# Optimization experiments

Hardware: AMD Instinct MI355X
Metric: run time of the kernel (lower is better)

## Reference

```python
import jax, jax.numpy as jnp
import numpy as np

N = 50000        # nodes
E = 800000       # edges (avg degree 16)
IN = 256         # in_size
H = 4            # heads
C = 32           # out_size per head
NEG_SLOPE = 0.2  # PyG GATConv leaky_relu slope
LN_EPS = 1e-5


def setup_inputs() -> dict:
    key = jax.random.key(0)
    ks = jax.random.split(key, 6)
    x = jax.random.normal(ks[0], (N, IN), dtype=jnp.float32)
    edge_index = jax.random.randint(ks[1], (2, E), 0, N, dtype=jnp.int32)
    W = jax.random.normal(ks[2], (IN, H * C), dtype=jnp.float32) * 0.05
    att_src = jax.random.normal(ks[3], (H, C), dtype=jnp.float32) * 0.05
    att_dst = jax.random.normal(ks[4], (H, C), dtype=jnp.float32) * 0.05
    bias = jnp.zeros((H * C,), dtype=jnp.float32)
    ln_gamma = jnp.ones((H * C,), dtype=jnp.float32)
    ln_beta = jnp.zeros((H * C,), dtype=jnp.float32)
    return {"x": x, "edge_index": edge_index, "W": W, "att_src": att_src,
            "att_dst": att_dst, "bias": bias, "ln_gamma": ln_gamma,
            "ln_beta": ln_beta}


def _segment_softmax(alpha, seg, num_segments):
    # alpha: [E, H], softmax over edges sharing the same destination node.
    amax = jax.ops.segment_max(alpha, seg, num_segments=num_segments)  # [N, H]
    amax = jnp.where(jnp.isfinite(amax), amax, 0.0)  # nodes with no in-edges
    ex = jnp.exp(alpha - amax[seg])
    denom = jax.ops.segment_sum(ex, seg, num_segments=num_segments)    # [N, H]
    return ex / (denom[seg] + 1e-16)


def reference(x, edge_index, W, att_src, att_dst, bias, ln_gamma, ln_beta):
    # --- GATConv (concat=True) ---
    x_lin = (x @ W).reshape(N, H, C)                    # [N, H, C]
    a_src = jnp.sum(x_lin * att_src, axis=-1)           # [N, H]
    a_dst = jnp.sum(x_lin * att_dst, axis=-1)           # [N, H]
    src, dst = edge_index[0], edge_index[1]             # messages src -> dst
    alpha = a_src[src] + a_dst[dst]                     # [E, H]
    alpha = jnp.where(alpha >= 0, alpha, NEG_SLOPE * alpha)
    alpha = _segment_softmax(alpha, dst, N)             # [E, H]
    msg = x_lin[src] * alpha[..., None]                 # [E, H, C]
    out = jax.ops.segment_sum(msg, dst, num_segments=N) # [N, H, C]
    out = out.reshape(N, H * C) + bias                  # [N, H*C]
    # --- LayerNorm over feature dim ---
    mu = jnp.mean(out, axis=-1, keepdims=True)
    var = jnp.mean(jnp.square(out - mu), axis=-1, keepdims=True)
    out = (out - mu) * jax.lax.rsqrt(var + LN_EPS) * ln_gamma + ln_beta
    # --- activation ---
    return jax.nn.relu(out)
```

## Files before the change

kernel.cpp:

```cpp
#include <hip/hip_runtime.h>

#define NNODES 50000
#define NEDGES 800000
#define INFEAT 256
#define HC 128
#define NH 4
#define CPH 32

typedef unsigned int uint32;
typedef unsigned short u16;
typedef short short8 __attribute__((ext_vector_type(8)));
typedef float f32x4 __attribute__((ext_vector_type(4)));

__device__ __forceinline__ float b2f(u16 s) {
    uint32 u = ((uint32)s) << 16;
    return __builtin_bit_cast(float, u);
}
__device__ __forceinline__ u16 f2bf(float x) {
    uint32 u = __builtin_bit_cast(uint32, x);
    uint32 r = (u + 0x7FFFu + ((u >> 16) & 1u)) >> 16;
    return (u16)r;
}
__device__ __forceinline__ uint32 pkh2(float a, float b) {
    _Float16 ha = (_Float16)a, hb = (_Float16)b;
    uint32 ua = (uint32)__builtin_bit_cast(unsigned short, ha);
    uint32 ub = (uint32)__builtin_bit_cast(unsigned short, hb);
    return ua | (ub << 16);
}
__device__ __forceinline__ float h2f(u16 h) {
    return (float)__builtin_bit_cast(_Float16, h);
}
__device__ __forceinline__ bool probe_bf16(const void* gamma) {
    return ((const uint32*)gamma)[0] == 0x3F803F80u;
}

__global__ __launch_bounds__(256) void wt_kernel(const void* __restrict__ W,
                                                 const void* __restrict__ gm,
                                                 u16* __restrict__ wt) {
    const bool isbf = probe_bf16(gm);
    int n = blockIdx.x;
    int k = threadIdx.x;
    u16 v;
    if (isbf) v = ((const u16*)W)[k * HC + n];
    else      v = f2bf(((const float*)W)[k * HC + n]);
    wt[n * INFEAT + k] = v;
}

__global__ __launch_bounds__(256) void gemm_mfma(const void* __restrict__ x,
                                                 const u16* __restrict__ wt,
                                                 const void* __restrict__ gm,
                                                 u16* __restrict__ xlin) {
    const bool isbf = probe_bf16(gm);
    int wave = blockIdx.x * 4 + (threadIdx.x >> 6);
    int lane = threadIdx.x & 63;
    int r = lane & 15;
    int quad = lane >> 4;
    int m0 = wave * 16;
    int arow = m0 + r;
    if (arow > NNODES - 1) arow = NNODES - 1;
    const size_t abase = (size_t)arow * INFEAT + quad * 8;

    f32x4 acc[8];
#pragma unroll
    for (int nt = 0; nt < 8; ++nt) acc[nt] = (f32x4){0.f, 0.f, 0.f, 0.f};

#pragma unroll
    for (int kt = 0; kt < 8; ++kt) {
        const int k0 = kt * 32;
        short8 afrag;
        if (isbf) {
            uint4 q = *(const uint4*)((const u16*)x + abase + k0);
            afrag = __builtin_bit_cast(short8, q);
        } else {
            const float* xp = (const float*)x + abase + k0;
            float4 f0 = *(const float4*)xp;
            float4 f1 = *(const float4*)(xp + 4);
            uint4 q;
            q.x = (uint32)f2bf(f0.x) | ((uint32)f2bf(f0.y) << 16);
            q.y = (uint32)f2bf(f0.z) | ((uint32)f2bf(f0.w) << 16);
            q.z = (uint32)f2bf(f1.x) | ((uint32)f2bf(f1.y) << 16);
            q.w = (uint32)f2bf(f1.z) | ((uint32)f2bf(f1.w) << 16);
            afrag = __builtin_bit_cast(short8, q);
        }
#pragma unroll
        for (int nt = 0; nt < 8; ++nt) {
            uint4 qb = *(const uint4*)(wt + (size_t)(nt * 16 + r) * INFEAT + k0 + quad * 8);
            short8 bfrag = __builtin_bit_cast(short8, qb);
            acc[nt] = __builtin_amdgcn_mfma_f32_16x16x32_bf16(afrag, bfrag, acc[nt], 0, 0, 0);
        }
    }
#pragma unroll
    for (int nt = 0; nt < 8; ++nt) {
#pragma unroll
        for (int reg = 0; reg < 4; ++reg) {
            int grow = m0 + quad * 4 + reg;
            if (grow < NNODES) xlin[(size_t)grow * HC + nt * 16 + r] = f2bf(acc[nt][reg]);
        }
    }
}

__global__ __launch_bounds__(256) void scores_kernel(const u16* __restrict__ xlin,
                                                     const void* __restrict__ att_src,
                                                     const void* __restrict__ att_dst,
                                                     const void* __restrict__ gm,
                                                     float* __restrict__ asrc,
                                                     float* __restrict__ adst) {
    const bool isbf = probe_bf16(gm);
    int idx = blockIdx.x * 256 + threadIdx.x;
    if (idx >= NNODES * NH) return;
    int n = idx >> 2, h = idx & 3;
    const u16* xp = xlin + (size_t)n * HC + h * CPH;

    float as[CPH], ad[CPH];
    if (isbf) {
#pragma unroll
        for (int q = 0; q < 4; q++) {
            uint4 va = *(const uint4*)((const u16*)att_src + h * CPH + q * 8);
            uint4 vd = *(const uint4*)((const u16*)att_dst + h * CPH + q * 8);
            const uint32 wa[4] = {va.x, va.y, va.z, va.w};
            const uint32 wd[4] = {vd.x, vd.y, vd.z, vd.w};
#pragma unroll
            for (int j = 0; j < 4; j++) {
                as[q * 8 + j * 2]     = b2f((u16)(wa[j] & 0xffffu));
                as[q * 8 + j * 2 + 1] = b2f((u16)(wa[j] >> 16));
                ad[q * 8 + j * 2]     = b2f((u16)(wd[j] & 0xffffu));
                ad[q * 8 + j * 2 + 1] = b2f((u16)(wd[j] >> 16));
            }
        }
    } else {
#pragma unroll
        for (int q = 0; q < 8; q++) {
            float4 va = *(const float4*)((const float*)att_src + h * CPH + q * 4);
            float4 vd = *(const float4*)((const float*)att_dst + h * CPH + q * 4);
            as[q * 4 + 0] = va.x; as[q * 4 + 1] = va.y; as[q * 4 + 2] = va.z; as[q * 4 + 3] = va.w;
            ad[q * 4 + 0] = vd.x; ad[q * 4 + 1] = vd.y; ad[q * 4 + 2] = vd.z; ad[q * 4 + 3] = vd.w;
        }
    }

    float ds = 0.f, dd = 0.f;
#pragma unroll
    for (int q = 0; q < 4; q++) {
        uint4 v = *(const uint4*)(xp + q * 8);
        const uint32 wv[4] = {v.x, v.y, v.z, v.w};
#pragma unroll
        for (int j = 0; j < 4; j++) {
            float x0 = b2f((u16)(wv[j] & 0xffffu));
            float x1 = b2f((u16)(wv[j] >> 16));
            int c = q * 8 + j * 2;
            ds = fmaf(x0, as[c], ds); ds = fmaf(x1, as[c + 1], ds);
            dd = fmaf(x0, ad[c], dd); dd = fmaf(x1, ad[c + 1], dd);
        }
    }
    asrc[idx] = ds;
    adst[idx] = dd;
}

__global__ __launch_bounds__(256) void hist_kernel(const int* __restrict__ ei,
                                                   int* __restrict__ count,
                                                   int* __restrict__ rank) {
    int e = blockIdx.x * 256 + threadIdx.x;
    if (e < NEDGES) rank[e] = atomicAdd(&count[ei[NEDGES + e]], 1);
}

__global__ __launch_bounds__(256) void blkred_kernel(const int* __restrict__ count,
                                                     int* __restrict__ blksum) {
    int i = blockIdx.x * 256 + threadIdx.x;
    int v = (i < NNODES) ? count[i] : 0;
#pragma unroll
    for (int m = 1; m < 64; m <<= 1) v += __shfl_xor(v, m);
    __shared__ int s[4];
    if ((threadIdx.x & 63) == 0) s[threadIdx.x >> 6] = v;
    __syncthreads();
    if (threadIdx.x == 0) blksum[blockIdx.x] = s[0] + s[1] + s[2] + s[3];
}

__global__ __launch_bounds__(256) void blkscan_kernel(const int* __restrict__ blksum,
                                                      int* __restrict__ base) {
    __shared__ int sd[256];
    int t = threadIdx.x;
    int nblk = (NNODES + 255) / 256;
    int v = (t < nblk) ? blksum[t] : 0;
    sd[t] = v;
    __syncthreads();
    for (int off = 1; off < 256; off <<= 1) {
        int tv = (t >= off) ? sd[t - off] : 0;
        __syncthreads();
        sd[t] += tv;
        __syncthreads();
    }
    if (t < nblk) base[t] = sd[t] - v;
}

__global__ __launch_bounds__(256) void scanout_kernel(const int* __restrict__ count,
                                                      const int* __restrict__ base,
                                                      int* __restrict__ offsets) {
    __shared__ int sd[256];
    int t = threadIdx.x;
    int i = blockIdx.x * 256 + t;
    int v = (i < NNODES) ? count[i] : 0;
    sd[t] = v;
    __syncthreads();
    for (int off = 1; off < 256; off <<= 1) {
        int tv = (t >= off) ? sd[t - off] : 0;
        __syncthreads();
        sd[t] += tv;
        __syncthreads();
    }
    if (i < NNODES) offsets[i] = base[blockIdx.x] + sd[t] - v;
    if (i == 0) offsets[NNODES] = NEDGES;
}

__global__ __launch_bounds__(256) void scatter_kernel(const int* __restrict__ ei,
                                                      const int* __restrict__ offsets,
                                                      const int* __restrict__ rank,
                                                      const float* __restrict__ asrc,
                                                      const float* __restrict__ adst,
                                                      uint4* __restrict__ recs) {
    int e = blockIdx.x * 256 + threadIdx.x;
    if (e >= NEDGES) return;
    int s = ei[e];
    int d = ei[NEDGES + e];
    int pos = offsets[d] + rank[e];
    float4 av = *(const float4*)(asrc + s * 4);
    float4 dv = *(const float4*)(adst + d * 4);
    float a0 = av.x + dv.x, a1 = av.y + dv.y, a2 = av.z + dv.z, a3 = av.w + dv.w;
    a0 = (a0 >= 0.f) ? a0 : 0.2f * a0;
    a1 = (a1 >= 0.f) ? a1 : 0.2f * a1;
    a2 = (a2 >= 0.f) ? a2 : 0.2f * a2;
    a3 = (a3 >= 0.f) ? a3 : 0.2f * a3;
    uint4 rec;
    rec.x = (uint32)s;
    rec.y = pkh2(__expf(a0), __expf(a1));
    rec.z = pkh2(__expf(a2), __expf(a3));
    rec.w = 0u;
    recs[pos] = rec;
}

__device__ __forceinline__ float recw(const uint4& r, int h) {
    uint32 wp = (h & 2) ? r.z : r.y;
    u16 wh = (h & 1) ? (u16)(wp >> 16) : (u16)(wp & 0xffffu);
    return h2f(wh);
}

__global__ __launch_bounds__(256) void node_kernel(const u16* __restrict__ xlin,
                                                   const int* __restrict__ offsets,
                                                   const uint4* __restrict__ recs,
                                                   const void* __restrict__ bias,
                                                   const void* __restrict__ gamma,
                                                   const void* __restrict__ beta,
                                                   void* __restrict__ out) {
    const bool isbf = probe_bf16(gamma);
    int node = blockIdx.x * 4 + (threadIdx.x >> 6);
    int lane = threadIdx.x & 63;
    int h = lane >> 4;
    int f2 = lane * 2;
    int start = offsets[node];
    int end = offsets[node + 1];

    float dsum = 0.f, acc0 = 0.f, acc1 = 0.f;
    int i = start;
    for (; i + 3 < end; i += 4) {
        uint4 r0 = recs[i + 0];
        uint4 r1 = recs[i + 1];
        uint4 r2 = recs[i + 2];
        uint4 r3 = recs[i + 3];
        float w0 = recw(r0, h), w1 = recw(r1, h), w2 = recw(r2, h), w3 = recw(r3, h);
        uint32 p0 = *(const uint32*)(xlin + (size_t)r0.x * HC + f2);
        uint32 p1 = *(const uint32*)(xlin + (size_t)r1.x * HC + f2);
        uint32 p2 = *(const uint32*)(xlin + (size_t)r2.x * HC + f2);
        uint32 p3 = *(const uint32*)(xlin + (size_t)r3.x * HC + f2);
        dsum += (w0 + w1) + (w2 + w3);
        acc0 = fmaf(b2f((u16)(p0 & 0xffffu)), w0, acc0);
        acc1 = fmaf(b2f((u16)(p0 >> 16)), w0, acc1);
        acc0 = fmaf(b2f((u16)(p1 & 0xffffu)), w1, acc0);
        acc1 = fmaf(b2f((u16)(p1 >> 16)), w1, acc1);
        acc0 = fmaf(b2f((u16)(p2 & 0xffffu)), w2, acc0);
        acc1 = fmaf(b2f((u16)(p2 >> 16)), w2, acc1);
        acc0 = fmaf(b2f((u16)(p3 & 0xffffu)), w3, acc0);
        acc1 = fmaf(b2f((u16)(p3 >> 16)), w3, acc1);
    }
    for (; i < end; ++i) {
        uint4 r = recs[i];
        float w = recw(r, h);
        uint32 p = *(const uint32*)(xlin + (size_t)r.x * HC + f2);
        dsum += w;
        acc0 = fmaf(b2f((u16)(p & 0xffffu)), w, acc0);
        acc1 = fmaf(b2f((u16)(p >> 16)), w, acc1);
    }
    float rden = 1.f / (dsum + 1e-16f);

    float bi0, bi1, g0, g1, be0, be1;
    if (isbf) {
        uint32 bb = ((const uint32*)bias)[lane];
        uint32 gg = ((const uint32*)gamma)[lane];
        uint32 eb = ((const uint32*)beta)[lane];
        bi0 = b2f((u16)(bb & 0xffffu)); bi1 = b2f((u16)(bb >> 16));
        g0  = b2f((u16)(gg & 0xffffu)); g1  = b2f((u16)(gg >> 16));
        be0 = b2f((u16)(eb & 0xffffu)); be1 = b2f((u16)(eb >> 16));
    } else {
        float2 tb = ((const float2*)bias)[lane];
        float2 tg = ((const float2*)gamma)[lane];
        float2 te = ((const float2*)beta)[lane];
        bi0 = tb.x; bi1 = tb.y; g0 = tg.x; g1 = tg.y; be0 = te.x; be1 = te.y;
    }
    float v0 = fmaf(acc0, rden, bi0);
    float v1 = fmaf(acc1, rden, bi1);
    float s2 = v0 + v1;
#pragma unroll
    for (int m = 1; m < 64; m <<= 1) s2 += __shfl_xor(s2, m);
    float mean = s2 * (1.f / 128.f);
    float d0 = v0 - mean, d1 = v1 - mean;
    float vv = d0 * d0 + d1 * d1;
#pragma unroll
    for (int m = 1; m < 64; m <<= 1) vv += __shfl_xor(vv, m);
    float inv = rsqrtf(vv * (1.f / 128.f) + 1e-5f);
    float o0 = fmaxf(fmaf(d0 * inv, g0, be0), 0.f);
    float o1 = fmaxf(fmaf(d1 * inv, g1, be1), 0.f);
    if (isbf) {
        uint32 po = (uint32)f2bf(o0) | ((uint32)f2bf(o1) << 16);
        ((uint32*)out)[(size_t)node * 64 + lane] = po;
    } else {
        float2 po; po.x = o0; po.y = o1;
        ((float2*)out)[(size_t)node * 64 + lane] = po;
    }
}

extern "C" void kernel_launch(void* const* d_in, const int* in_sizes, int n_in,
                              void* d_out, int out_size, void* d_ws, size_t ws_size,
                              hipStream_t stream) {
    const void* x       = d_in[0];
    const int*  ei      = (const int*)d_in[1];
    const void* W       = d_in[2];
    const void* att_src = d_in[3];
    const void* att_dst = d_in[4];
    const void* bias    = d_in[5];
    const void* gamma   = d_in[6];
    const void* beta    = d_in[7];

    char* w = (char*)d_ws;
    size_t off = 0;
    u16* xlin    = (u16*)(w + off);   off += 12800000;
    u16* wt      = (u16*)(w + off);   off += 65536;
    float* asrc  = (float*)(w + off); off += 800000;
    float* adst  = (float*)(w + off); off += 800000;
    int* count   = (int*)(w + off);   off += 200000;
    int* offsets = (int*)(w + off);   off += 200016;
    int* rank    = (int*)(w + off);   off += 3200000;
    int* blksum  = (int*)(w + off);   off += 1024;
    int* base    = (int*)(w + off);   off += 1024;
    uint4* recs  = (uint4*)(w + off); off += 12800000;

    hipMemsetAsync(count, 0, 200000, stream);

    const int NBLK = (NNODES + 255) / 256;
    wt_kernel<<<HC, 256, 0, stream>>>(W, gamma, wt);
    gemm_mfma<<<(NNODES + 63) / 64, 256, 0, stream>>>(x, wt, gamma, xlin);
    scores_kernel<<<(NNODES * NH + 255) / 256, 256, 0, stream>>>(xlin, att_src, att_dst, gamma, asrc, adst);
    hist_kernel<<<(NEDGES + 255) / 256, 256, 0, stream>>>(ei, count, rank);
    blkred_kernel<<<NBLK, 256, 0, stream>>>(count, blksum);
    blkscan_kernel<<<1, 256, 0, stream>>>(blksum, base);
    scanout_kernel<<<NBLK, 256, 0, stream>>>(count, base, offsets);
    scatter_kernel<<<(NEDGES + 255) / 256, 256, 0, stream>>>(ei, offsets, rank, asrc, adst, recs);
    node_kernel<<<NNODES / 4, 256, 0, stream>>>(xlin, offsets, recs, bias, gamma, beta, d_out);
}
```

Baseline: 253.6 us.

## Fuse attention scores into GEMM, merge scan kernels, drop memset, deepen gather unroll

The per-head attention dot products are now computed from the GEMM accumulators inside the MFMA kernel using cross-lane shuffles, which removes the separate scores kernel and its re-read of xlin. The count buffer is zeroed inside the weight transpose kernel instead of by a memset. The block-level scan is folded into the scanout kernel, with every block redundantly scanning the block sums. The node kernel's edge gather is unrolled to 8, and LayerNorm uses a single-pass sum and sum-of-squares reduction, which trades some numerical stability for fewer shuffles.

```diff
diff --git a/kernel.cpp b/kernel.cpp
--- a/kernel.cpp
+++ b/kernel.cpp
@@ -36,7 +36,8 @@
 
 __global__ __launch_bounds__(256) void wt_kernel(const void* __restrict__ W,
                                                  const void* __restrict__ gm,
-                                                 u16* __restrict__ wt) {
+                                                 u16* __restrict__ wt,
+                                                 int* __restrict__ count) {
     const bool isbf = probe_bf16(gm);
     int n = blockIdx.x;
     int k = threadIdx.x;
@@ -44,12 +45,18 @@
     if (isbf) v = ((const u16*)W)[k * HC + n];
     else      v = f2bf(((const float*)W)[k * HC + n]);
     wt[n * INFEAT + k] = v;
+    int tid = blockIdx.x * 256 + threadIdx.x;
+    for (int i = tid; i < NNODES; i += HC * 256) count[i] = 0;
 }
 
 __global__ __launch_bounds__(256) void gemm_mfma(const void* __restrict__ x,
                                                  const u16* __restrict__ wt,
+                                                 const void* __restrict__ att_src,
+                                                 const void* __restrict__ att_dst,
                                                  const void* __restrict__ gm,
-                                                 u16* __restrict__ xlin) {
+                                                 u16* __restrict__ xlin,
+                                                 float* __restrict__ asrc,
+                                                 float* __restrict__ adst) {
     const bool isbf = probe_bf16(gm);
     int wave = blockIdx.x * 4 + (threadIdx.x >> 6);
     int lane = threadIdx.x & 63;
@@ -97,62 +104,54 @@
             if (grow < NNODES) xlin[(size_t)grow * HC + nt * 16 + r] = f2bf(acc[nt][reg]);
         }
     }
-}
-
-__global__ __launch_bounds__(256) void scores_kernel(const u16* __restrict__ xlin,
-                                                     const void* __restrict__ att_src,
-                                                     const void* __restrict__ att_dst,
-                                                     const void* __restrict__ gm,
-                                                     float* __restrict__ asrc,
-                                                     float* __restrict__ adst) {
-    const bool isbf = probe_bf16(gm);
-    int idx = blockIdx.x * 256 + threadIdx.x;
-    if (idx >= NNODES * NH) return;
-    int n = idx >> 2, h = idx & 3;
-    const u16* xp = xlin + (size_t)n * HC + h * CPH;
-
-    float as[CPH], ad[CPH];
-    if (isbf) {
-#pragma unroll
-        for (int q = 0; q < 4; q++) {
-            uint4 va = *(const uint4*)((const u16*)att_src + h * CPH + q * 8);
-            uint4 vd = *(const uint4*)((const u16*)att_dst + h * CPH + q * 8);
-            const uint32 wa[4] = {va.x, va.y, va.z, va.w};
-            const uint32 wd[4] = {vd.x, vd.y, vd.z, vd.w};
-#pragma unroll
-            for (int j = 0; j < 4; j++) {
-                as[q * 8 + j * 2]     = b2f((u16)(wa[j] & 0xffffu));
-                as[q * 8 + j * 2 + 1] = b2f((u16)(wa[j] >> 16));
-                ad[q * 8 + j * 2]     = b2f((u16)(wd[j] & 0xffffu));
-                ad[q * 8 + j * 2 + 1] = b2f((u16)(wd[j] >> 16));
+
+    float asv[8], adv[8];
+#pragma unroll
+    for (int nt = 0; nt < 8; ++nt) {
+        int c = nt * 16 + r;
+        if (isbf) {
+            asv[nt] = b2f(((const u16*)att_src)[c]);
+            adv[nt] = b2f(((const u16*)att_dst)[c]);
+        } else {
+            asv[nt] = ((const float*)att_src)[c];
+            adv[nt] = ((const float*)att_dst)[c];
+        }
+    }
+    float psrc[4][4], pdst[4][4];
+#pragma unroll
+    for (int h = 0; h < 4; ++h)
+#pragma unroll
+        for (int reg = 0; reg < 4; ++reg) { psrc[h][reg] = 0.f; pdst[h][reg] = 0.f; }
+#pragma unroll
+    for (int nt = 0; nt < 8; ++nt) {
+        const int h = nt >> 1;
+#pragma unroll
+        for (int reg = 0; reg < 4; ++reg) {
+            psrc[h][reg] = fmaf(acc[nt][reg], asv[nt], psrc[h][reg]);
+            pdst[h][reg] = fmaf(acc[nt][reg], adv[nt], pdst[h][reg]);
+        }
+    }
+#pragma unroll
+    for (int m = 1; m < 16; m <<= 1) {
+#pragma unroll
+        for (int h = 0; h < 4; ++h)
+#pragma unroll
+            for (int reg = 0; reg < 4; ++reg) {
+                psrc[h][reg] += __shfl_xor(psrc[h][reg], m);
+                pdst[h][reg] += __shfl_xor(pdst[h][reg], m);
             }
-        }
-    } else {
-#pragma unroll
-        for (int q = 0; q < 8; q++) {
-            float4 va = *(const float4*)((const float*)att_src + h * CPH + q * 4);
-            float4 vd = *(const float4*)((const float*)att_dst + h * CPH + q * 4);
-            as[q * 4 + 0] = va.x; as[q * 4 + 1] = va.y; as[q * 4 + 2] = va.z; as[q * 4 + 3] = va.w;
-            ad[q * 4 + 0] = vd.x; ad[q * 4 + 1] = vd.y; ad[q * 4 + 2] = vd.z; ad[q * 4 + 3] = vd.w;
-        }
-    }
-
-    float ds = 0.f, dd = 0.f;
-#pragma unroll
-    for (int q = 0; q < 4; q++) {
-        uint4 v = *(const uint4*)(xp + q * 8);
-        const uint32 wv[4] = {v.x, v.y, v.z, v.w};
-#pragma unroll
-        for (int j = 0; j < 4; j++) {
-            float x0 = b2f((u16)(wv[j] & 0xffffu));
-            float x1 = b2f((u16)(wv[j] >> 16));
-            int c = q * 8 + j * 2;
-            ds = fmaf(x0, as[c], ds); ds = fmaf(x1, as[c + 1], ds);
-            dd = fmaf(x0, ad[c], dd); dd = fmaf(x1, ad[c + 1], dd);
-        }
-    }
-    asrc[idx] = ds;
-    adst[idx] = dd;
+    }
+#pragma unroll
+    for (int reg = 0; reg < 4; ++reg)
+#pragma unroll
+        for (int h = 0; h < 4; ++h)
+            if (r == reg * 4 + h) {
+                int grow = m0 + quad * 4 + reg;
+                if (grow < NNODES) {
+                    asrc[grow * 4 + h] = psrc[h][reg];
+                    adst[grow * 4 + h] = pdst[h][reg];
+                }
+            }
 }
 
 __global__ __launch_bounds__(256) void hist_kernel(const int* __restrict__ ei,
@@ -174,28 +173,24 @@
     if (threadIdx.x == 0) blksum[blockIdx.x] = s[0] + s[1] + s[2] + s[3];
 }
 
-__global__ __launch_bounds__(256) void blkscan_kernel(const int* __restrict__ blksum,
-                                                      int* __restrict__ base) {
+__global__ __launch_bounds__(256) void scanout_kernel(const int* __restrict__ count,
+                                                      const int* __restrict__ blksum,
+                                                      int* __restrict__ offsets) {
+    __shared__ int sb[256];
     __shared__ int sd[256];
+    const int nblk = (NNODES + 255) / 256;
     int t = threadIdx.x;
-    int nblk = (NNODES + 255) / 256;
-    int v = (t < nblk) ? blksum[t] : 0;
-    sd[t] = v;
+    int bv = (t < nblk) ? blksum[t] : 0;
+    sb[t] = bv;
     __syncthreads();
     for (int off = 1; off < 256; off <<= 1) {
-        int tv = (t >= off) ? sd[t - off] : 0;
+        int tv = (t >= off) ? sb[t - off] : 0;
         __syncthreads();
-        sd[t] += tv;
+        sb[t] += tv;
         __syncthreads();
     }
-    if (t < nblk) base[t] = sd[t] - v;
-}
-
-__global__ __launch_bounds__(256) void scanout_kernel(const int* __restrict__ count,
-                                                      const int* __restrict__ base,
-                                                      int* __restrict__ offsets) {
-    __shared__ int sd[256];
-    int t = threadIdx.x;
+    int base = sb[blockIdx.x] - blksum[blockIdx.x];
+
     int i = blockIdx.x * 256 + t;
     int v = (i < NNODES) ? count[i] : 0;
     sd[t] = v;
@@ -206,7 +201,7 @@
         sd[t] += tv;
         __syncthreads();
     }
-    if (i < NNODES) offsets[i] = base[blockIdx.x] + sd[t] - v;
+    if (i < NNODES) offsets[i] = base + sd[t] - v;
     if (i == 0) offsets[NNODES] = NEDGES;
 }
 
@@ -259,25 +254,35 @@
 
     float dsum = 0.f, acc0 = 0.f, acc1 = 0.f;
     int i = start;
+    for (; i + 7 < end; i += 8) {
+        uint4 rr[8];
+        uint32 pp[8];
+#pragma unroll
+        for (int j = 0; j < 8; ++j) rr[j] = recs[i + j];
+#pragma unroll
+        for (int j = 0; j < 8; ++j) pp[j] = *(const uint32*)(xlin + (size_t)rr[j].x * HC + f2);
+#pragma unroll
+        for (int j = 0; j < 8; ++j) {
+            float w = recw(rr[j], h);
+            dsum += w;
+            acc0 = fmaf(b2f((u16)(pp[j] & 0xffffu)), w, acc0);
+            acc1 = fmaf(b2f((u16)(pp[j] >> 16)), w, acc1);
+        }
+    }
     for (; i + 3 < end; i += 4) {
-        uint4 r0 = recs[i + 0];
-        uint4 r1 = recs[i + 1];
-        uint4 r2 = recs[i + 2];
-        uint4 r3 = recs[i + 3];
-        float w0 = recw(r0, h), w1 = recw(r1, h), w2 = recw(r2, h), w3 = recw(r3, h);
-        uint32 p0 = *(const uint32*)(xlin + (size_t)r0.x * HC + f2);
-        uint32 p1 = *(const uint32*)(xlin + (size_t)r1.x * HC + f2);
-        uint32 p2 = *(const uint32*)(xlin + (size_t)r2.x * HC + f2);
-        uint32 p3 = *(const uint32*)(xlin + (size_t)r3.x * HC + f2);
-        dsum += (w0 + w1) + (w2 + w3);
-        acc0 = fmaf(b2f((u16)(p0 & 0xffffu)), w0, acc0);
-        acc1 = fmaf(b2f((u16)(p0 >> 16)), w0, acc1);
-        acc0 = fmaf(b2f((u16)(p1 & 0xffffu)), w1, acc0);
-        acc1 = fmaf(b2f((u16)(p1 >> 16)), w1, acc1);
-        acc0 = fmaf(b2f((u16)(p2 & 0xffffu)), w2, acc0);
-        acc1 = fmaf(b2f((u16)(p2 >> 16)), w2, acc1);
-        acc0 = fmaf(b2f((u16)(p3 & 0xffffu)), w3, acc0);
-        acc1 = fmaf(b2f((u16)(p3 >> 16)), w3, acc1);
+        uint4 rr[4];
+        uint32 pp[4];
+#pragma unroll
+        for (int j = 0; j < 4; ++j) rr[j] = recs[i + j];
+#pragma unroll
+        for (int j = 0; j < 4; ++j) pp[j] = *(const uint32*)(xlin + (size_t)rr[j].x * HC + f2);
+#pragma unroll
+        for (int j = 0; j < 4; ++j) {
+            float w = recw(rr[j], h);
+            dsum += w;
+            acc0 = fmaf(b2f((u16)(pp[j] & 0xffffu)), w, acc0);
+            acc1 = fmaf(b2f((u16)(pp[j] >> 16)), w, acc1);
+        }
     }
     for (; i < end; ++i) {
         uint4 r = recs[i];
@@ -306,14 +311,16 @@
     float v0 = fmaf(acc0, rden, bi0);
     float v1 = fmaf(acc1, rden, bi1);
     float s2 = v0 + v1;
-#pragma unroll
-    for (int m = 1; m < 64; m <<= 1) s2 += __shfl_xor(s2, m);
+    float q2 = v0 * v0 + v1 * v1;
+#pragma unroll
+    for (int m = 1; m < 64; m <<= 1) {
+        s2 += __shfl_xor(s2, m);
+        q2 += __shfl_xor(q2, m);
+    }
     float mean = s2 * (1.f / 128.f);
+    float var = q2 * (1.f / 128.f) - mean * mean;
+    float inv = rsqrtf(var + 1e-5f);
     float d0 = v0 - mean, d1 = v1 - mean;
-    float vv = d0 * d0 + d1 * d1;
-#pragma unroll
-    for (int m = 1; m < 64; m <<= 1) vv += __shfl_xor(vv, m);
-    float inv = rsqrtf(vv * (1.f / 128.f) + 1e-5f);
     float o0 = fmaxf(fmaf(d0 * inv, g0, be0), 0.f);
     float o1 = fmaxf(fmaf(d1 * inv, g1, be1), 0.f);
     if (isbf) {
@@ -347,19 +354,15 @@
     int* offsets = (int*)(w + off);   off += 200016;
     int* rank    = (int*)(w + off);   off += 3200000;
     int* blksum  = (int*)(w + off);   off += 1024;
-    int* base    = (int*)(w + off);   off += 1024;
     uint4* recs  = (uint4*)(w + off); off += 12800000;
 
-    hipMemsetAsync(count, 0, 200000, stream);
-
     const int NBLK = (NNODES + 255) / 256;
-    wt_kernel<<<HC, 256, 0, stream>>>(W, gamma, wt);
-    gemm_mfma<<<(NNODES + 63) / 64, 256, 0, stream>>>(x, wt, gamma, xlin);
-    scores_kernel<<<(NNODES * NH + 255) / 256, 256, 0, stream>>>(xlin, att_src, att_dst, gamma, asrc, adst);
+    wt_kernel<<<HC, 256, 0, stream>>>(W, gamma, wt, count);
+    gemm_mfma<<<(NNODES + 63) / 64, 256, 0, stream>>>(x, wt, att_src, att_dst, gamma,
+                                                      xlin, asrc, adst);
     hist_kernel<<<(NEDGES + 255) / 256, 256, 0, stream>>>(ei, count, rank);
     blkred_kernel<<<NBLK, 256, 0, stream>>>(count, blksum);
-    blkscan_kernel<<<1, 256, 0, stream>>>(blksum, base);
-    scanout_kernel<<<NBLK, 256, 0, stream>>>(count, base, offsets);
+    scanout_kernel<<<NBLK, 256, 0, stream>>>(count, blksum, offsets);
     scatter_kernel<<<(NEDGES + 255) / 256, 256, 0, stream>>>(ei, offsets, rank, asrc, adst, recs);
     node_kernel<<<NNODES / 4, 256, 0, stream>>>(xlin, offsets, recs, bias, gamma, beta, d_out);
 }
```

Measured after the change: 243.1 us. -4.1%, faster.
